# Kernel tuning notes

Measured on AMD Instinct MI355X. Metric: run time of the kernel, lower is better.

Reference implementation:

```python
import jax, jax.numpy as jnp
import numpy as np

B, S, D, DS, NSLOT = 2, 1024, 1024, 320, 512
H, CH = 4, 5
DFF = 4 * D
MAXIT = 2


def _ln(x, g, b, eps=1e-5):
    m = x.mean(-1, keepdims=True)
    v = ((x - m) ** 2).mean(-1, keepdims=True)
    return (x - m) * jax.lax.rsqrt(v + eps) * g + b


def _mha(x, Wq, Wk, Wv, Wo, bq, bk, bv, bo, nh):
    b_, s_, d_ = x.shape
    hd = d_ // nh
    q = (x @ Wq + bq).reshape(b_, s_, nh, hd)
    k = (x @ Wk + bk).reshape(b_, s_, nh, hd)
    v = (x @ Wv + bv).reshape(b_, s_, nh, hd)
    a = jax.nn.softmax(jnp.einsum('bqhd,bkhd->bhqk', q, k) * (hd ** -0.5), axis=-1)
    o = jnp.einsum('bhqk,bkhd->bqhd', a, v).reshape(b_, s_, d_)
    return o @ Wo + bo


def setup_inputs():
    key = jax.random.key(0)
    ks = iter(jax.random.split(key, 64))
    n = lambda shape: jax.random.normal(next(ks), shape, jnp.float32) * 0.02
    z = lambda shape: jnp.zeros(shape, jnp.float32)
    o = lambda shape: jnp.ones(shape, jnp.float32)
    return dict(
        x=jax.random.normal(next(ks), (B, S, D), jnp.float32),
        cache=jax.random.normal(next(ks), (B, NSLOT, DS), jnp.float32),
        iter_emb=n((16, D)),
        rq_w=n((D, D)), rg_w=n((D, 1)), rg_b=z((1,)), ck_w=n((DS, D)), cv_w=n((DS, D)),
        aq_w=n((D, D)), ak_w=n((D, D)), av_w=n((D, D)), ao_w=n((D, D)),
        aq_b=z((D,)), ak_b=z((D,)), av_b=z((D,)), ao_b=z((D,)),
        f1_w=n((D, DFF)), f1_b=z((DFF,)), f2_w=n((DFF, D)), f2_b=z((D,)),
        n1_g=o((D,)), n1_b=z((D,)), n2_g=o((D,)), n2_b=z((D,)),
        sq_w=n((DS, DS)), tk_w=n((D, DS)), tv_w=n((D, DS)), wg_w=n((D, 1)), wg_b=z((1,)),
        cq_w=n((DS, DS)), ck2_w=n((DS, DS)), cv2_w=n((DS, DS)), co_w=n((DS, DS)),
        cq_b=z((DS,)), ck2_b=z((DS,)), cv2_b=z((DS,)), co_b=z((DS,)),
        cn_g=o((DS,)), cn_b=z((DS,)),
        max_iterations=MAXIT,
    )


def reference(x, cache, iter_emb, rq_w, rg_w, rg_b, ck_w, cv_w,
              aq_w, ak_w, av_w, ao_w, aq_b, ak_b, av_b, ao_b,
              f1_w, f1_b, f2_w, f2_b, n1_g, n1_b, n2_g, n2_b,
              sq_w, tk_w, tv_w, wg_w, wg_b,
              cq_w, ck2_w, cv2_w, co_w, cq_b, ck2_b, cv2_b, co_b, cn_g, cn_b,
              max_iterations):
    def mem_read(h, cc):
        # gather from cache: gated cross-attention readout
        q = h @ rq_w                                   # [B,S,D]
        k = cc @ ck_w                                  # [B,N,D]
        v = cc @ cv_w                                  # [B,N,D]
        a = jax.nn.softmax(jnp.einsum('bsd,bnd->bsn', q, k) * (D ** -0.5), axis=-1)
        readout = jnp.einsum('bsn,bnd->bsd', a, v)
        gate = jax.nn.sigmoid(h @ rg_w + rg_b)          # [B,S,1] soft read gate
        return h + gate * readout

    def compute_block(h):
        # faithful to ComputeBlock (non-linear-attention branch): norm1 used twice
        hn = _ln(h, n1_g, n1_b)
        attn = _mha(hn, aq_w, ak_w, av_w, ao_w, aq_b, ak_b, av_b, ao_b, H)
        h = _ln(h + attn, n1_g, n1_b)
        ffn = jax.nn.gelu(h @ f1_w + f1_b) @ f2_w + f2_b
        return _ln(h + ffn, n2_g, n2_b)

    def mem_write(h, cc):
        # importance-scored scatter: slots attend over tokens, gated by importance
        sq = cc @ sq_w                                  # [B,N,DS]
        tk = h @ tk_w                                   # [B,S,DS]
        tv = h @ tv_w                                   # [B,S,DS]
        gate = jax.nn.sigmoid(h @ wg_w + wg_b)          # [B,S,1] soft write gate
        a = jax.nn.softmax(jnp.einsum('bnd,bsd->bns', sq, tk) * (DS ** -0.5), axis=-1)
        upd = jnp.einsum('bns,bsd->bnd', a, gate * tv)
        return cc + upd

    def cache_self_attn(cc):
        attn = _mha(cc, cq_w, ck2_w, cv2_w, co_w, cq_b, ck2_b, cv2_b, co_b, CH)
        return _ln(cc + attn, cn_g, cn_b)

    h = x
    cc = cache
    layer_input = x
    h_prev = None
    for it in range(max_iterations):
        h = h + iter_emb[it][None, None, :]
        if it > 0:
            h = h + layer_input + h_prev
        h_enh = mem_read(h, cc)
        h_comp = compute_block(h_enh)
        cc = mem_write(h_comp, cc)
        cc = cache_self_attn(cc)
        h = h_comp
        h_prev = jax.lax.stop_gradient(h_comp)  # torch: h_prev = h_computed.detach()
    return h
```

## Files before the change

### kernel.cpp

```cpp
#include <hip/hip_runtime.h>
#include <cstdint>

constexpr int B_ = 2, S_ = 1024, D_ = 1024, DS_ = 320, NSLOT_ = 512;
constexpr int H_ = 4, CH_ = 5, DFF_ = 4096;
constexpr int HD_ = D_ / H_;
constexpr int CHD_ = DS_ / CH_;
constexpr int BS_ = B_ * S_;
constexpr int BNS_ = B_ * NSLOT_;

typedef unsigned short u16;
typedef __attribute__((ext_vector_type(8))) short bf16x8;
typedef __attribute__((ext_vector_type(4))) float f32x4;
typedef __attribute__((ext_vector_type(4))) u16 u16x4;
typedef long long ll;

__device__ __forceinline__ u16 f2bf(float f) {
  unsigned u = __float_as_uint(f);
  return (u16)((u + 0x7FFFu + ((u >> 16) & 1u)) >> 16);
}
__device__ __forceinline__ float bf2f(u16 h) { return __uint_as_float((unsigned)h << 16); }

__device__ __forceinline__ void gload16(const void* g, void* l) {
  __builtin_amdgcn_global_load_lds((const __attribute__((address_space(1))) void*)g,
                                   (__attribute__((address_space(3))) void*)l, 16, 0, 0);
}

__global__ __launch_bounds__(512, 4)
void k_gemm(const u16* __restrict__ A, int lda, ll sA, ll sA2,
            const u16* __restrict__ Bp, int ldb, ll sB, ll sB2,
            float* __restrict__ outF, u16* __restrict__ outB,
            int ldc, ll sC, ll sC2,
            u16* __restrict__ outBT, int ldt, ll sT, ll sT2,
            int K, int zdiv, const float* __restrict__ bias,
            const float* __restrict__ rowscale, int rscfrom,
            int splitcol, int act)
{
  constexpr int ABYT = 128 * 128;
  constexpr int BBYT = 64 * 128;
  constexpr int BUF = ABYT + BBYT;
  const int z = blockIdx.z, zb = z / zdiv, zr = z - zb * zdiv;
  A  += (ll)zb * sA + (ll)zr * sA2;
  Bp += (ll)zb * sB + (ll)zr * sB2;
  const ll cof = (ll)zb * sC + (ll)zr * sC2;
  const ll tof = (ll)zb * sT + (ll)zr * sT2;
  const int bm = blockIdx.y * 128, bn = blockIdx.x * 64;
  __shared__ __align__(16) char lds[3 * BUF];
  const int tid = threadIdx.x;
  const int lane = tid & 63, wid = tid >> 6;
  const int rowb = wid * 16;

  f32x4 acc[4];
  const f32x4 fz = {0.f, 0.f, 0.f, 0.f};
  #pragma unroll
  for (int j = 0; j < 4; ++j) acc[j] = fz;

  const int trow = tid >> 3;
  const int tg   = ((tid & 7) ^ (trow & 7)) * 8;
  const u16* gA  = A + (ll)(bm + trow) * lda + tg;
  const u16* gA2 = gA + (ll)64 * lda;
  const u16* gB  = Bp + (ll)(bn + trow) * ldb + tg;

  const int r = lane & 15, q = lane >> 4;
  const int c7 = r & 7;
  const int gs0 = ((q) ^ c7) << 4;
  const int gs1 = ((4 + q) ^ c7) << 4;
  const int aoff = (rowb + r) * 128;
  int boff[4];
  #pragma unroll
  for (int j = 0; j < 4; ++j) boff[j] = ABYT + (j * 16 + r) * 128;

  auto stage = [&](int buf, int it) {
    char* la = lds + buf * BUF + wid * 1024;
    char* lb = la + ABYT;
    const int ko = it << 6;
    gload16(gA + ko, la);
    gload16(gA2 + ko, la + 8192);
    gload16(gB + ko, lb);
  };

  const int nsteps = K >> 6;
  stage(0, 0);
  if (nsteps > 1) stage(1, 1);
  for (int it = 0; it < nsteps; ++it) {
    if (it == nsteps - 1) asm volatile("s_waitcnt vmcnt(0)" ::: "memory");
    else                  asm volatile("s_waitcnt vmcnt(3)" ::: "memory");
    __builtin_amdgcn_s_barrier();
    __builtin_amdgcn_sched_barrier(0);
    if (it + 2 < nsteps) {
      int nb = it + 2; while (nb >= 3) nb -= 3;
      stage(nb, it + 2);
    }
    int p = it; while (p >= 3) p -= 3;
    const char* pa = lds + p * BUF;
    #pragma unroll
    for (int s = 0; s < 2; ++s) {
      const int gso = s ? gs1 : gs0;
      bf16x8 af = *(const bf16x8*)(pa + aoff + gso);
      bf16x8 bv[4];
      #pragma unroll
      for (int j = 0; j < 4; ++j) bv[j] = *(const bf16x8*)(pa + boff[j] + gso);
      #pragma unroll
      for (int j = 0; j < 4; ++j)
        acc[j] = __builtin_amdgcn_mfma_f32_16x16x32_bf16(af, bv[j], acc[j], 0, 0, 0);
    }
    asm volatile("s_waitcnt lgkmcnt(0)" ::: "memory");
    __builtin_amdgcn_sched_barrier(0);
  }

  const int fr = lane & 15, fq = lane >> 4;
  const int r0 = bm + rowb + fq * 4;
  #pragma unroll
  for (int j = 0; j < 4; ++j) {
    const int cn = bn + j * 16 + fr;
    const float bvv = bias ? bias[cn] : 0.f;
    const bool doRs = rowscale && (cn >= rscfrom);
    float vv[4];
    #pragma unroll
    for (int t = 0; t < 4; ++t) {
      float v = acc[j][t] + bvv;
      if (doRs) v *= rowscale[r0 + t];
      if (act) v = 0.5f * v * (1.f + tanhf(0.7978845608028654f * (v + 0.044715f * v * v * v)));
      vv[t] = v;
    }
    if (cn < splitcol) {
      if (outF) {
        #pragma unroll
        for (int t = 0; t < 4; ++t) outF[cof + (ll)(r0 + t) * ldc + cn] = vv[t];
      }
      if (outB) {
        #pragma unroll
        for (int t = 0; t < 4; ++t) outB[cof + (ll)(r0 + t) * ldc + cn] = f2bf(vv[t]);
      }
    } else {
      u16x4 pk = {f2bf(vv[0]), f2bf(vv[1]), f2bf(vv[2]), f2bf(vv[3])};
      *(u16x4*)(outBT + tof + (ll)(cn - splitcol) * ldt + r0) = pk;
    }
  }
}

struct PrepTable {
  const float* src[16];
  u16* dst[16];
  int R[16];
  int C[16];
  int off[17];
};

__global__ __launch_bounds__(256)
void k_prep_all(PrepTable T)
{
  __shared__ float t[32][33];
  const int b = blockIdx.x;
  int w = 0;
  #pragma unroll
  for (int i = 1; i < 16; ++i) if (b >= T.off[i]) w = i;
  const int lb = b - T.off[w];
  const int tilesC = T.C[w] >> 5;
  const int by = (lb / tilesC) << 5;
  const int bx = (lb - (lb / tilesC) * tilesC) << 5;
  const float* in = T.src[w];
  u16* out = T.dst[w];
  const int R = T.R[w], C = T.C[w];
  const int tx = threadIdx.x & 31, ty = threadIdx.x >> 5;
  #pragma unroll
  for (int i = 0; i < 32; i += 8)
    t[ty + i][tx] = in[(ll)(by + ty + i) * C + bx + tx];
  __syncthreads();
  #pragma unroll
  for (int i = 0; i < 32; i += 8)
    out[(ll)(bx + ty + i) * R + by + tx] = f2bf(t[tx][ty + i]);
}

__global__ __launch_bounds__(256)
void k_cvt(const float* __restrict__ in, u16* __restrict__ out, int n)
{
  int i = blockIdx.x * 256 + threadIdx.x;
  if (i < n) out[i] = f2bf(in[i]);
}

__global__ __launch_bounds__(256)
void k_cat3f(float* __restrict__ dst, const float* __restrict__ a, int na,
             const float* __restrict__ b, int nb, const float* __restrict__ c, int nc)
{
  int i = blockIdx.x * 256 + threadIdx.x;
  if (i < na) dst[i] = a[i];
  else if (i < na + nb) dst[i] = b[i - na];
  else if (i < na + nb + nc) dst[i] = c[i - na - nb];
}

__global__ __launch_bounds__(256)
void k_softmax_b16(u16* __restrict__ x, int cols, float scale)
{
  u16* p = x + (ll)blockIdx.x * cols;
  const int tid = threadIdx.x;
  __shared__ float red[256];
  float v[4];
  float m = -1e30f;
  #pragma unroll
  for (int i = 0; i < 4; ++i) {
    const int c = tid + (i << 8);
    v[i] = (c < cols) ? bf2f(p[c]) * scale : -1e30f;
    m = fmaxf(m, v[i]);
  }
  red[tid] = m; __syncthreads();
  for (int s = 128; s > 0; s >>= 1) { if (tid < s) red[tid] = fmaxf(red[tid], red[tid + s]); __syncthreads(); }
  m = red[0]; __syncthreads();
  float sum = 0.f;
  #pragma unroll
  for (int i = 0; i < 4; ++i) { v[i] = expf(v[i] - m); sum += v[i]; }
  red[tid] = sum; __syncthreads();
  for (int s = 128; s > 0; s >>= 1) { if (tid < s) red[tid] += red[tid + s]; __syncthreads(); }
  const float inv = 1.f / red[0];
  #pragma unroll
  for (int i = 0; i < 4; ++i) {
    const int c = tid + (i << 8);
    if (c < cols) p[c] = f2bf(v[i] * inv);
  }
}

__global__ __launch_bounds__(256)
void k_layernorm(const float* __restrict__ x, const float* __restrict__ res,
                 const float* __restrict__ res2, const float* __restrict__ rbias,
                 const float* __restrict__ g, const float* __restrict__ b,
                 float* __restrict__ outF, u16* __restrict__ outB, int cols)
{
  const ll ro = (ll)blockIdx.x * cols;
  const float* px = x + ro;
  const float* pr = res ? res + ro : nullptr;
  const float* p2 = res2 ? res2 + ro : nullptr;
  __shared__ float red[256];
  const int tid = threadIdx.x;
  auto val = [&](int c) {
    float v = px[c];
    if (pr) v += pr[c];
    if (p2) v += p2[c];
    if (rbias) v += rbias[c];
    return v;
  };
  float s = 0.f;
  for (int c = tid; c < cols; c += 256) s += val(c);
  red[tid] = s; __syncthreads();
  for (int t = 128; t > 0; t >>= 1) { if (tid < t) red[tid] += red[tid + t]; __syncthreads(); }
  const float mean = red[0] / cols; __syncthreads();
  float s2 = 0.f;
  for (int c = tid; c < cols; c += 256) { float v = val(c) - mean; s2 += v * v; }
  red[tid] = s2; __syncthreads();
  for (int t = 128; t > 0; t >>= 1) { if (tid < t) red[tid] += red[tid + t]; __syncthreads(); }
  const float inv = rsqrtf(red[0] / cols + 1e-5f);
  for (int c = tid; c < cols; c += 256) {
    float v = (val(c) - mean) * inv * g[c] + b[c];
    if (outF) outF[ro + c] = v;
    if (outB) outB[ro + c] = f2bf(v);
  }
}

__global__ __launch_bounds__(256)
void k_gate_add_ln(const float* __restrict__ h, const float* __restrict__ rr,
                   const float* __restrict__ w, const float* __restrict__ b0,
                   const float* __restrict__ g, const float* __restrict__ b,
                   float* __restrict__ outF, u16* __restrict__ outB)
{
  constexpr int C = 1024;
  const ll ro = (ll)blockIdx.x * C;
  const float* ph = h + ro;
  const float* pr = rr + ro;
  __shared__ float red[256];
  const int tid = threadIdx.x;
  float hv[4], rv[4];
  float s = 0.f;
  #pragma unroll
  for (int i = 0; i < 4; ++i) {
    const int c = tid + (i << 8);
    hv[i] = ph[c]; rv[i] = pr[c];
    s += hv[i] * w[c];
  }
  red[tid] = s; __syncthreads();
  for (int t = 128; t > 0; t >>= 1) { if (tid < t) red[tid] += red[tid + t]; __syncthreads(); }
  const float gate = 1.0f / (1.0f + expf(-(red[0] + b0[0])));
  __syncthreads();
  float vsum = 0.f;
  float vv[4];
  #pragma unroll
  for (int i = 0; i < 4; ++i) { vv[i] = hv[i] + gate * rv[i]; vsum += vv[i]; }
  red[tid] = vsum; __syncthreads();
  for (int t = 128; t > 0; t >>= 1) { if (tid < t) red[tid] += red[tid + t]; __syncthreads(); }
  const float mean = red[0] / C; __syncthreads();
  float v2 = 0.f;
  #pragma unroll
  for (int i = 0; i < 4; ++i) { float d = vv[i] - mean; v2 += d * d; }
  red[tid] = v2; __syncthreads();
  for (int t = 128; t > 0; t >>= 1) { if (tid < t) red[tid] += red[tid + t]; __syncthreads(); }
  const float inv = rsqrtf(red[0] / C + 1e-5f);
  #pragma unroll
  for (int i = 0; i < 4; ++i) {
    const int c = tid + (i << 8);
    outF[ro + c] = vv[i];
    outB[ro + c] = f2bf((vv[i] - mean) * inv * g[c] + b[c]);
  }
}

__global__ __launch_bounds__(256)
void k_gate(const float* __restrict__ x, const float* __restrict__ w,
            const float* __restrict__ b0, float* __restrict__ out, int cols)
{
  const int lane = threadIdx.x & 63;
  const int wv = threadIdx.x >> 6;
  const ll row = (ll)blockIdx.x * 4 + wv;
  const float* p = x + row * cols;
  float s = 0.f;
  for (int c = lane; c < cols; c += 64) s += p[c] * w[c];
  #pragma unroll
  for (int off = 32; off > 0; off >>= 1) s += __shfl_down(s, off);
  if (lane == 0) out[row] = 1.0f / (1.0f + expf(-(s + b0[0])));
}

__global__ __launch_bounds__(256)
void k_combine2(float* __restrict__ oF, u16* __restrict__ oB,
                const float* __restrict__ a, float sa, const float* __restrict__ b,
                const float* __restrict__ emb, int n, int Dm1)
{
  int i = blockIdx.x * 256 + threadIdx.x;
  if (i >= n) return;
  float v = sa * a[i];
  if (b) v += b[i];
  v += emb[i & Dm1];
  oF[i] = v; oB[i] = f2bf(v);
}

__global__ __launch_bounds__(256)
void k_add2(float* __restrict__ oF, u16* __restrict__ oB,
            const float* __restrict__ a, const float* __restrict__ b, int n)
{
  int i = blockIdx.x * 256 + threadIdx.x;
  if (i >= n) return;
  float v = a[i] + b[i];
  oF[i] = v; oB[i] = f2bf(v);
}

extern "C" void kernel_launch(void* const* d_in, const int* in_sizes, int n_in,
                              void* d_out, int out_size, void* d_ws, size_t ws_size,
                              hipStream_t stream)
{
  (void)in_sizes; (void)n_in; (void)out_size;
  const float* x        = (const float*)d_in[0];
  const float* cache0   = (const float*)d_in[1];
  const float* iter_emb = (const float*)d_in[2];
  const float* rq_w     = (const float*)d_in[3];
  const float* rg_w     = (const float*)d_in[4];
  const float* rg_b     = (const float*)d_in[5];
  const float* ck_w     = (const float*)d_in[6];
  const float* cv_w     = (const float*)d_in[7];
  const float* aq_w     = (const float*)d_in[8];
  const float* ak_w     = (const float*)d_in[9];
  const float* av_w     = (const float*)d_in[10];
  const float* ao_w     = (const float*)d_in[11];
  const float* aq_b     = (const float*)d_in[12];
  const float* ak_b     = (const float*)d_in[13];
  const float* av_b     = (const float*)d_in[14];
  const float* ao_b     = (const float*)d_in[15];
  const float* f1_w     = (const float*)d_in[16];
  const float* f1_b     = (const float*)d_in[17];
  const float* f2_w     = (const float*)d_in[18];
  const float* f2_b     = (const float*)d_in[19];
  const float* n1_g     = (const float*)d_in[20];
  const float* n1_b     = (const float*)d_in[21];
  const float* n2_g     = (const float*)d_in[22];
  const float* n2_b     = (const float*)d_in[23];
  const float* sq_w     = (const float*)d_in[24];
  const float* tk_w     = (const float*)d_in[25];
  const float* tv_w     = (const float*)d_in[26];
  const float* wg_w     = (const float*)d_in[27];
  const float* wg_b     = (const float*)d_in[28];
  const float* cq_w     = (const float*)d_in[29];
  const float* ck2_w    = (const float*)d_in[30];
  const float* cv2_w    = (const float*)d_in[31];
  const float* co_w     = (const float*)d_in[32];
  const float* cq_b     = (const float*)d_in[33];
  const float* ck2_b    = (const float*)d_in[34];
  const float* cv2_b    = (const float*)d_in[35];
  const float* co_b     = (const float*)d_in[36];
  const float* cn_g     = (const float*)d_in[37];
  const float* cn_b     = (const float*)d_in[38];

  float* out = (float*)d_out;

  size_t off = 0;
  char* base = (char*)d_ws;
  auto allocF = [&](size_t n) { float* p = (float*)(base + off); off += n * 4; off = (off + 255) & ~(size_t)255; return p; };
  auto allocH = [&](size_t n) { u16* p = (u16*)(base + off); off += n * 2; off = (off + 255) & ~(size_t)255; return p; };

  float* hbuf  = allocF((size_t)BS_ * D_);
  float* henh  = allocF((size_t)BS_ * D_);
  float* hcomp = allocF((size_t)BS_ * D_);
  float* h2b   = allocF((size_t)BS_ * D_);
  float* tA    = allocF((size_t)2 * BS_ * D_);
  float* gate  = allocF((size_t)BS_);
  float* ccnf  = allocF((size_t)BNS_ * DS_);
  float* updf  = allocF((size_t)BNS_ * DS_);
  float* coo   = allocF((size_t)BNS_ * DS_);
  float* ccwf  = allocF((size_t)BNS_ * DS_);
  float* qkvb  = allocF(3 * D_);
  float* cqkvb = allocF(3 * DS_);
  u16* rqT  = allocH((size_t)D_ * D_);
  u16* ckT  = allocH((size_t)D_ * DS_);
  u16* cvT  = allocH((size_t)D_ * DS_);
  u16* aqT  = allocH((size_t)D_ * D_);
  u16* akT  = allocH((size_t)D_ * D_);
  u16* avT  = allocH((size_t)D_ * D_);
  u16* aoT  = allocH((size_t)D_ * D_);
  u16* f1T  = allocH((size_t)DFF_ * D_);
  u16* f2T  = allocH((size_t)D_ * DFF_);
  u16* sqT  = allocH((size_t)DS_ * DS_);
  u16* tkT  = allocH((size_t)DS_ * D_);
  u16* tvTw = allocH((size_t)DS_ * D_);
  u16* cqT  = allocH((size_t)DS_ * DS_);
  u16* ck2T = allocH((size_t)DS_ * DS_);
  u16* cv2T = allocH((size_t)DS_ * DS_);
  u16* coT  = allocH((size_t)DS_ * DS_);
  u16* bb1  = allocH((size_t)BS_ * D_);
  u16* bb2  = allocH((size_t)BS_ * D_);
  u16* bb3  = allocH((size_t)BS_ * D_);
  u16* bb4  = allocH((size_t)BS_ * D_);
  u16* bb5  = allocH((size_t)B_ * H_ * S_ * S_);
  u16* bbQK = allocH((size_t)BS_ * 2 * D_);
  u16* bbCQK= allocH((size_t)BNS_ * 2 * DS_);
  u16* cc0b = allocH((size_t)BNS_ * DS_);
  u16* ccwb = allocH((size_t)BNS_ * DS_);
  u16* sqb  = allocH((size_t)BNS_ * DS_);
  u16* tkb  = allocH((size_t)BS_ * DS_);
  u16* tvTb = allocH((size_t)DS_ * BS_);
  u16* ccnb = allocH((size_t)BNS_ * DS_);
  u16* cv2Tb= allocH((size_t)DS_ * BNS_);
  u16* csab = allocH((size_t)BNS_ * DS_);
  if (off > ws_size) return;
  (void)cvT; (void)akT; (void)avT; (void)tvTw; (void)ck2T; (void)cv2T;

  auto gemm = [&](int M, int N, int K, int z, int zdiv,
                  const u16* Ap, int lda, ll sa, ll sa2,
                  const u16* Bq, int ldb, ll sb, ll sb2,
                  float* oF, u16* oB, int ldc, ll sc, ll sc2,
                  u16* oBT, int ldt, ll st, ll st2,
                  const float* bias, const float* rsc, int rscfrom,
                  int splitcol, int act) {
    dim3 g(N / 64, M / 128, z);
    k_gemm<<<g, 512, 0, stream>>>(Ap, lda, sa, sa2, Bq, ldb, sb, sb2,
        oF, oB, ldc, sc, sc2, oBT, ldt, st, st2, K, zdiv, bias, rsc, rscfrom, splitcol, act);
  };
  auto lnorm = [&](const float* xp, const float* rp, const float* rp2, const float* rb,
                   const float* g, const float* b, float* oF, u16* oB, int rows, int cols) {
    k_layernorm<<<rows, 256, 0, stream>>>(xp, rp, rp2, rb, g, b, oF, oB, cols);
  };
  auto eg = [](int n) { return dim3((n + 255) / 256); };

  {
    PrepTable T;
    const float* srcs[16] = {rq_w, ck_w, cv_w, aq_w, ak_w, av_w, ao_w, f1_w,
                             f2_w, sq_w, tk_w, tv_w, cq_w, ck2_w, cv2_w, co_w};
    u16* dsts[16] = {rqT, ckT, cvT, aqT, akT, avT, aoT, f1T,
                     f2T, sqT, tkT, tvTw, cqT, ck2T, cv2T, coT};
    const int Rs[16] = {D_, DS_, DS_, D_, D_, D_, D_, D_, DFF_, DS_, D_, D_, DS_, DS_, DS_, DS_};
    const int Cs[16] = {D_, D_, D_, D_, D_, D_, D_, DFF_, D_, DS_, DS_, DS_, DS_, DS_, DS_, DS_};
    int acc0 = 0;
    for (int i = 0; i < 16; ++i) {
      T.src[i] = srcs[i]; T.dst[i] = dsts[i]; T.R[i] = Rs[i]; T.C[i] = Cs[i];
      T.off[i] = acc0;
      acc0 += (Rs[i] >> 5) * (Cs[i] >> 5);
    }
    T.off[16] = acc0;
    k_prep_all<<<acc0, 256, 0, stream>>>(T);
  }
  k_cvt<<<eg(BNS_ * DS_), 256, 0, stream>>>(cache0, cc0b, BNS_ * DS_);
  k_cat3f<<<eg(3 * D_), 256, 0, stream>>>(qkvb, aq_b, D_, ak_b, D_, av_b, D_);
  k_cat3f<<<eg(3 * DS_), 256, 0, stream>>>(cqkvb, cq_b, DS_, ck2_b, DS_, cv2_b, DS_);

  auto mem_read = [&](const float* h_f, const u16* h_b, const u16* cc_b, float* o_henh) {
    gemm(BS_, D_, D_, 1, 1, h_b, D_, 0, 0, rqT, D_, 0, 0,
         nullptr, bb2, D_, 0, 0, nullptr, 0, 0, 0,
         nullptr, nullptr, 0, D_, 0);
    gemm(BNS_, 2 * D_, DS_, 1, 1, cc_b, DS_, 0, 0, ckT, DS_, 0, 0,
         nullptr, bb3, D_, 0, 0, bb4, BNS_, 0, 0,
         nullptr, nullptr, 0, D_, 0);
    gemm(S_, NSLOT_, D_, B_, 1, bb2, D_, (ll)S_ * D_, 0,
         bb3, D_, (ll)NSLOT_ * D_, 0,
         nullptr, bb5, NSLOT_, (ll)S_ * NSLOT_, 0, nullptr, 0, 0, 0,
         nullptr, nullptr, 0, NSLOT_, 0);
    k_softmax_b16<<<B_ * S_, 256, 0, stream>>>(bb5, NSLOT_, 0.03125f);
    gemm(S_, D_, NSLOT_, B_, 1, bb5, NSLOT_, (ll)S_ * NSLOT_, 0,
         bb4, BNS_, NSLOT_, 0,
         tA, nullptr, D_, (ll)S_ * D_, 0, nullptr, 0, 0, 0,
         nullptr, nullptr, 0, D_, 0);
    k_gate_add_ln<<<BS_, 256, 0, stream>>>(h_f, tA, rg_w, rg_b, n1_g, n1_b,
                                           o_henh, bb1);
  };

  auto compute_block = [&](const float* he, float* oF, u16* oB) {
    gemm(BS_, 3 * D_, D_, 1, 1, bb1, D_, 0, 0, aqT, D_, 0, 0,
         nullptr, bbQK, 2 * D_, 0, 0, bb4, BS_, 0, 0,
         qkvb, nullptr, 0, 2 * D_, 0);
    gemm(S_, S_, HD_, B_ * H_, H_,
         bbQK, 2 * D_, (ll)S_ * 2 * D_, HD_,
         bbQK + D_, 2 * D_, (ll)S_ * 2 * D_, HD_,
         nullptr, bb5, S_, (ll)H_ * S_ * S_, (ll)S_ * S_, nullptr, 0, 0, 0,
         nullptr, nullptr, 0, S_, 0);
    k_softmax_b16<<<B_ * H_ * S_, 256, 0, stream>>>(bb5, S_, 0.0625f);
    gemm(S_, HD_, S_, B_ * H_, H_,
         bb5, S_, (ll)H_ * S_ * S_, (ll)S_ * S_,
         bb4, BS_, S_, (ll)HD_ * BS_,
         nullptr, bb2, D_, (ll)S_ * D_, HD_, nullptr, 0, 0, 0,
         nullptr, nullptr, 0, HD_, 0);
    gemm(BS_, D_, D_, 1, 1, bb2, D_, 0, 0, aoT, D_, 0, 0,
         tA, nullptr, D_, 0, 0, nullptr, 0, 0, 0,
         ao_b, nullptr, 0, D_, 0);
    lnorm(he, tA, nullptr, nullptr, n1_g, n1_b, h2b, bb1, BS_, D_);
    gemm(BS_, DFF_, D_, 1, 1, bb1, D_, 0, 0, f1T, D_, 0, 0,
         nullptr, bb5, DFF_, 0, 0, nullptr, 0, 0, 0,
         f1_b, nullptr, 0, DFF_, 1);
    gemm(BS_, D_, 2048, 2, 2, bb5, DFF_, 0, 2048, f2T, DFF_, 0, 2048,
         tA, nullptr, D_, 0, (ll)BS_ * D_, nullptr, 0, 0, 0,
         nullptr, nullptr, 0, D_, 0);
    lnorm(h2b, tA, tA + (ll)BS_ * D_, f2_b, n2_g, n2_b, oF, oB, BS_, D_);
  };

  auto mem_write_csa = [&](const float* hc_f, const u16* hc_b,
                           const float* ccin_f, const u16* ccin_b) {
    gemm(BNS_, DS_, DS_, 1, 1, ccin_b, DS_, 0, 0, sqT, DS_, 0, 0,
         nullptr, sqb, DS_, 0, 0, nullptr, 0, 0, 0,
         nullptr, nullptr, 0, DS_, 0);
    k_gate<<<BS_ / 4, 256, 0, stream>>>(hc_f, wg_w, wg_b, gate, D_);
    gemm(BS_, 2 * DS_, D_, 1, 1, hc_b, D_, 0, 0, tkT, D_, 0, 0,
         nullptr, tkb, DS_, 0, 0, tvTb, BS_, 0, 0,
         nullptr, gate, DS_, DS_, 0);
    gemm(NSLOT_, S_, DS_, B_, 1, sqb, DS_, (ll)NSLOT_ * DS_, 0,
         tkb, DS_, (ll)S_ * DS_, 0,
         nullptr, bb5, S_, (ll)NSLOT_ * S_, 0, nullptr, 0, 0, 0,
         nullptr, nullptr, 0, S_, 0);
    k_softmax_b16<<<B_ * NSLOT_, 256, 0, stream>>>(bb5, S_, 0.05590169943749474f);
    gemm(NSLOT_, DS_, S_, B_, 1, bb5, S_, (ll)NSLOT_ * S_, 0,
         tvTb, BS_, S_, 0,
         updf, nullptr, DS_, (ll)NSLOT_ * DS_, 0, nullptr, 0, 0, 0,
         nullptr, nullptr, 0, DS_, 0);
    k_add2<<<eg(BNS_ * DS_), 256, 0, stream>>>(ccnf, ccnb, ccin_f, updf, BNS_ * DS_);
    gemm(BNS_, 3 * DS_, DS_, 1, 1, ccnb, DS_, 0, 0, cqT, DS_, 0, 0,
         nullptr, bbCQK, 2 * DS_, 0, 0, cv2Tb, BNS_, 0, 0,
         cqkvb, nullptr, 0, 2 * DS_, 0);
    gemm(NSLOT_, NSLOT_, CHD_, B_ * CH_, CH_,
         bbCQK, 2 * DS_, (ll)NSLOT_ * 2 * DS_, CHD_,
         bbCQK + DS_, 2 * DS_, (ll)NSLOT_ * 2 * DS_, CHD_,
         nullptr, bb5, NSLOT_, (ll)CH_ * NSLOT_ * NSLOT_, (ll)NSLOT_ * NSLOT_,
         nullptr, 0, 0, 0, nullptr, nullptr, 0, NSLOT_, 0);
    k_softmax_b16<<<B_ * CH_ * NSLOT_, 256, 0, stream>>>(bb5, NSLOT_, 0.125f);
    gemm(NSLOT_, CHD_, NSLOT_, B_ * CH_, CH_,
         bb5, NSLOT_, (ll)CH_ * NSLOT_ * NSLOT_, (ll)NSLOT_ * NSLOT_,
         cv2Tb, BNS_, NSLOT_, (ll)CHD_ * BNS_,
         nullptr, csab, DS_, (ll)NSLOT_ * DS_, CHD_, nullptr, 0, 0, 0,
         nullptr, nullptr, 0, CHD_, 0);
    gemm(BNS_, DS_, DS_, 1, 1, csab, DS_, 0, 0, coT, DS_, 0, 0,
         coo, nullptr, DS_, 0, 0, nullptr, 0, 0, 0,
         co_b, nullptr, 0, DS_, 0);
    lnorm(ccnf, coo, nullptr, nullptr, cn_g, cn_b, ccwf, ccwb, BNS_, DS_);
  };

  k_combine2<<<eg(BS_ * D_), 256, 0, stream>>>(hbuf, bb1, x, 1.0f, nullptr, iter_emb, BS_ * D_, D_ - 1);
  mem_read(hbuf, bb1, cc0b, henh);
  compute_block(henh, hcomp, bb3);
  mem_write_csa(hcomp, bb3, cache0, cc0b);

  k_combine2<<<eg(BS_ * D_), 256, 0, stream>>>(hbuf, bb1, hcomp, 2.0f, x, iter_emb + D_, BS_ * D_, D_ - 1);
  mem_read(hbuf, bb1, ccwb, henh);
  compute_block(henh, out, nullptr);
}
```

Before: 530.0 us.

## Shrink GEMM tile to 64x64 with double buffering and fuse residual add

The GEMM kernel moves from 128x64 tiles with 512 threads and a 3-stage LDS ring to 64x64 tiles with 256 threads and 2-stage double buffering. The waitcnt drops to vmcnt(0) every step. This raises the block count for the small-M GEMMs (512- and 1024-row problems) and lowers LDS per block, but each block reuses less data and overlaps less load with compute. Separately, the cache-update residual add (k_add2) is folded into the attention-output GEMM epilogue through a new addF pointer, which removes one kernel launch and one intermediate buffer.

```diff
diff --git a/kernel.cpp b/kernel.cpp
--- a/kernel.cpp
+++ b/kernel.cpp
@@ -25,7 +25,7 @@
                                    (__attribute__((address_space(3))) void*)l, 16, 0, 0);
 }
 
-__global__ __launch_bounds__(512, 4)
+__global__ __launch_bounds__(256, 5)
 void k_gemm(const u16* __restrict__ A, int lda, ll sA, ll sA2,
             const u16* __restrict__ Bp, int ldb, ll sB, ll sB2,
             float* __restrict__ outF, u16* __restrict__ outB,
@@ -33,9 +33,10 @@
             u16* __restrict__ outBT, int ldt, ll sT, ll sT2,
             int K, int zdiv, const float* __restrict__ bias,
             const float* __restrict__ rowscale, int rscfrom,
+            const float* __restrict__ addF,
             int splitcol, int act)
 {
-  constexpr int ABYT = 128 * 128;
+  constexpr int ABYT = 64 * 128;
   constexpr int BBYT = 64 * 128;
   constexpr int BUF = ABYT + BBYT;
   const int z = blockIdx.z, zb = z / zdiv, zr = z - zb * zdiv;
@@ -43,8 +44,8 @@
   Bp += (ll)zb * sB + (ll)zr * sB2;
   const ll cof = (ll)zb * sC + (ll)zr * sC2;
   const ll tof = (ll)zb * sT + (ll)zr * sT2;
-  const int bm = blockIdx.y * 128, bn = blockIdx.x * 64;
-  __shared__ __align__(16) char lds[3 * BUF];
+  const int bm = blockIdx.y * 64, bn = blockIdx.x * 64;
+  __shared__ __align__(16) char lds[2 * BUF];
   const int tid = threadIdx.x;
   const int lane = tid & 63, wid = tid >> 6;
   const int rowb = wid * 16;
@@ -57,8 +58,9 @@
   const int trow = tid >> 3;
   const int tg   = ((tid & 7) ^ (trow & 7)) * 8;
   const u16* gA  = A + (ll)(bm + trow) * lda + tg;
-  const u16* gA2 = gA + (ll)64 * lda;
+  const u16* gA2 = gA + (ll)32 * lda;
   const u16* gB  = Bp + (ll)(bn + trow) * ldb + tg;
+  const u16* gB2 = gB + (ll)32 * ldb;
 
   const int r = lane & 15, q = lane >> 4;
   const int c7 = r & 7;
@@ -74,24 +76,20 @@
     char* lb = la + ABYT;
     const int ko = it << 6;
     gload16(gA + ko, la);
-    gload16(gA2 + ko, la + 8192);
+    gload16(gA2 + ko, la + 4096);
     gload16(gB + ko, lb);
+    gload16(gB2 + ko, lb + 4096);
   };
 
   const int nsteps = K >> 6;
   stage(0, 0);
-  if (nsteps > 1) stage(1, 1);
+  int bufp = 0;
   for (int it = 0; it < nsteps; ++it) {
-    if (it == nsteps - 1) asm volatile("s_waitcnt vmcnt(0)" ::: "memory");
-    else                  asm volatile("s_waitcnt vmcnt(3)" ::: "memory");
+    asm volatile("s_waitcnt vmcnt(0)" ::: "memory");
     __builtin_amdgcn_s_barrier();
     __builtin_amdgcn_sched_barrier(0);
-    if (it + 2 < nsteps) {
-      int nb = it + 2; while (nb >= 3) nb -= 3;
-      stage(nb, it + 2);
-    }
-    int p = it; while (p >= 3) p -= 3;
-    const char* pa = lds + p * BUF;
+    if (it + 1 < nsteps) stage(bufp ^ 1, it + 1);
+    const char* pa = lds + bufp * BUF;
     #pragma unroll
     for (int s = 0; s < 2; ++s) {
       const int gso = s ? gs1 : gs0;
@@ -105,6 +103,7 @@
     }
     asm volatile("s_waitcnt lgkmcnt(0)" ::: "memory");
     __builtin_amdgcn_sched_barrier(0);
+    bufp ^= 1;
   }
 
   const int fr = lane & 15, fq = lane >> 4;
@@ -120,6 +119,7 @@
       float v = acc[j][t] + bvv;
       if (doRs) v *= rowscale[r0 + t];
       if (act) v = 0.5f * v * (1.f + tanhf(0.7978845608028654f * (v + 0.044715f * v * v * v)));
+      if (addF) v += addF[cof + (ll)(r0 + t) * ldc + cn];
       vv[t] = v;
     }
     if (cn < splitcol) {
@@ -324,16 +324,6 @@
   float v = sa * a[i];
   if (b) v += b[i];
   v += emb[i & Dm1];
-  oF[i] = v; oB[i] = f2bf(v);
-}
-
-__global__ __launch_bounds__(256)
-void k_add2(float* __restrict__ oF, u16* __restrict__ oB,
-            const float* __restrict__ a, const float* __restrict__ b, int n)
-{
-  int i = blockIdx.x * 256 + threadIdx.x;
-  if (i >= n) return;
-  float v = a[i] + b[i];
   oF[i] = v; oB[i] = f2bf(v);
 }
 
@@ -396,7 +386,6 @@
   float* tA    = allocF((size_t)2 * BS_ * D_);
   float* gate  = allocF((size_t)BS_);
   float* ccnf  = allocF((size_t)BNS_ * DS_);
-  float* updf  = allocF((size_t)BNS_ * DS_);
   float* coo   = allocF((size_t)BNS_ * DS_);
   float* ccwf  = allocF((size_t)BNS_ * DS_);
   float* qkvb  = allocF(3 * D_);
@@ -441,10 +430,11 @@
                   float* oF, u16* oB, int ldc, ll sc, ll sc2,
                   u16* oBT, int ldt, ll st, ll st2,
                   const float* bias, const float* rsc, int rscfrom,
-                  int splitcol, int act) {
-    dim3 g(N / 64, M / 128, z);
-    k_gemm<<<g, 512, 0, stream>>>(Ap, lda, sa, sa2, Bq, ldb, sb, sb2,
-        oF, oB, ldc, sc, sc2, oBT, ldt, st, st2, K, zdiv, bias, rsc, rscfrom, splitcol, act);
+                  const float* addF, int splitcol, int act) {
+    dim3 g(N / 64, M / 64, z);
+    k_gemm<<<g, 256, 0, stream>>>(Ap, lda, sa, sa2, Bq, ldb, sb, sb2,
+        oF, oB, ldc, sc, sc2, oBT, ldt, st, st2, K, zdiv, bias, rsc, rscfrom,
+        addF, splitcol, act);
   };
   auto lnorm = [&](const float* xp, const float* rp, const float* rp2, const float* rb,
                    const float* g, const float* b, float* oF, u16* oB, int rows, int cols) {
@@ -476,19 +466,19 @@
   auto mem_read = [&](const float* h_f, const u16* h_b, const u16* cc_b, float* o_henh) {
     gemm(BS_, D_, D_, 1, 1, h_b, D_, 0, 0, rqT, D_, 0, 0,
          nullptr, bb2, D_, 0, 0, nullptr, 0, 0, 0,
-         nullptr, nullptr, 0, D_, 0);
+         nullptr, nullptr, 0, nullptr, D_, 0);
     gemm(BNS_, 2 * D_, DS_, 1, 1, cc_b, DS_, 0, 0, ckT, DS_, 0, 0,
          nullptr, bb3, D_, 0, 0, bb4, BNS_, 0, 0,
-         nullptr, nullptr, 0, D_, 0);
+         nullptr, nullptr, 0, nullptr, D_, 0);
     gemm(S_, NSLOT_, D_, B_, 1, bb2, D_, (ll)S_ * D_, 0,
          bb3, D_, (ll)NSLOT_ * D_, 0,
          nullptr, bb5, NSLOT_, (ll)S_ * NSLOT_, 0, nullptr, 0, 0, 0,
-         nullptr, nullptr, 0, NSLOT_, 0);
+         nullptr, nullptr, 0, nullptr, NSLOT_, 0);
     k_softmax_b16<<<B_ * S_, 256, 0, stream>>>(bb5, NSLOT_, 0.03125f);
     gemm(S_, D_, NSLOT_, B_, 1, bb5, NSLOT_, (ll)S_ * NSLOT_, 0,
          bb4, BNS_, NSLOT_, 0,
          tA, nullptr, D_, (ll)S_ * D_, 0, nullptr, 0, 0, 0,
-         nullptr, nullptr, 0, D_, 0);
+         nullptr, nullptr, 0, nullptr, D_, 0);
     k_gate_add_ln<<<BS_, 256, 0, stream>>>(h_f, tA, rg_w, rg_b, n1_g, n1_b,
                                            o_henh, bb1);
   };
@@ -496,28 +486,28 @@
   auto compute_block = [&](const float* he, float* oF, u16* oB) {
     gemm(BS_, 3 * D_, D_, 1, 1, bb1, D_, 0, 0, aqT, D_, 0, 0,
          nullptr, bbQK, 2 * D_, 0, 0, bb4, BS_, 0, 0,
-         qkvb, nullptr, 0, 2 * D_, 0);
+         qkvb, nullptr, 0, nullptr, 2 * D_, 0);
     gemm(S_, S_, HD_, B_ * H_, H_,
          bbQK, 2 * D_, (ll)S_ * 2 * D_, HD_,
          bbQK + D_, 2 * D_, (ll)S_ * 2 * D_, HD_,
          nullptr, bb5, S_, (ll)H_ * S_ * S_, (ll)S_ * S_, nullptr, 0, 0, 0,
-         nullptr, nullptr, 0, S_, 0);
+         nullptr, nullptr, 0, nullptr, S_, 0);
     k_softmax_b16<<<B_ * H_ * S_, 256, 0, stream>>>(bb5, S_, 0.0625f);
     gemm(S_, HD_, S_, B_ * H_, H_,
          bb5, S_, (ll)H_ * S_ * S_, (ll)S_ * S_,
          bb4, BS_, S_, (ll)HD_ * BS_,
          nullptr, bb2, D_, (ll)S_ * D_, HD_, nullptr, 0, 0, 0,
-         nullptr, nullptr, 0, HD_, 0);
+         nullptr, nullptr, 0, nullptr, HD_, 0);
     gemm(BS_, D_, D_, 1, 1, bb2, D_, 0, 0, aoT, D_, 0, 0,
          tA, nullptr, D_, 0, 0, nullptr, 0, 0, 0,
-         ao_b, nullptr, 0, D_, 0);
+         ao_b, nullptr, 0, nullptr, D_, 0);
     lnorm(he, tA, nullptr, nullptr, n1_g, n1_b, h2b, bb1, BS_, D_);
     gemm(BS_, DFF_, D_, 1, 1, bb1, D_, 0, 0, f1T, D_, 0, 0,
          nullptr, bb5, DFF_, 0, 0, nullptr, 0, 0, 0,
-         f1_b, nullptr, 0, DFF_, 1);
+         f1_b, nullptr, 0, nullptr, DFF_, 1);
     gemm(BS_, D_, 2048, 2, 2, bb5, DFF_, 0, 2048, f2T, DFF_, 0, 2048,
          tA, nullptr, D_, 0, (ll)BS_ * D_, nullptr, 0, 0, 0,
-         nullptr, nullptr, 0, D_, 0);
+         nullptr, nullptr, 0, nullptr, D_, 0);
     lnorm(h2b, tA, tA + (ll)BS_ * D_, f2_b, n2_g, n2_b, oF, oB, BS_, D_);
   };
 
@@ -525,38 +515,37 @@
                            const float* ccin_f, const u16* ccin_b) {
     gemm(BNS_, DS_, DS_, 1, 1, ccin_b, DS_, 0, 0, sqT, DS_, 0, 0,
          nullptr, sqb, DS_, 0, 0, nullptr, 0, 0, 0,
-         nullptr, nullptr, 0, DS_, 0);
+         nullptr, nullptr, 0, nullptr, DS_, 0);
     k_gate<<<BS_ / 4, 256, 0, stream>>>(hc_f, wg_w, wg_b, gate, D_);
     gemm(BS_, 2 * DS_, D_, 1, 1, hc_b, D_, 0, 0, tkT, D_, 0, 0,
          nullptr, tkb, DS_, 0, 0, tvTb, BS_, 0, 0,
-         nullptr, gate, DS_, DS_, 0);
+         nullptr, gate, DS_, nullptr, DS_, 0);
     gemm(NSLOT_, S_, DS_, B_, 1, sqb, DS_, (ll)NSLOT_ * DS_, 0,
          tkb, DS_, (ll)S_ * DS_, 0,
          nullptr, bb5, S_, (ll)NSLOT_ * S_, 0, nullptr, 0, 0, 0,
-         nullptr, nullptr, 0, S_, 0);
+         nullptr, nullptr, 0, nullptr, S_, 0);
     k_softmax_b16<<<B_ * NSLOT_, 256, 0, stream>>>(bb5, S_, 0.05590169943749474f);
     gemm(NSLOT_, DS_, S_, B_, 1, bb5, S_, (ll)NSLOT_ * S_, 0,
          tvTb, BS_, S_, 0,
-         updf, nullptr, DS_, (ll)NSLOT_ * DS_, 0, nullptr, 0, 0, 0,
-         nullptr, nullptr, 0, DS_, 0);
-    k_add2<<<eg(BNS_ * DS_), 256, 0, stream>>>(ccnf, ccnb, ccin_f, updf, BNS_ * DS_);
+         ccnf, ccnb, DS_, (ll)NSLOT_ * DS_, 0, nullptr, 0, 0, 0,
+         nullptr, nullptr, 0, ccin_f, DS_, 0);
     gemm(BNS_, 3 * DS_, DS_, 1, 1, ccnb, DS_, 0, 0, cqT, DS_, 0, 0,
          nullptr, bbCQK, 2 * DS_, 0, 0, cv2Tb, BNS_, 0, 0,
-         cqkvb, nullptr, 0, 2 * DS_, 0);
+         cqkvb, nullptr, 0, nullptr, 2 * DS_, 0);
     gemm(NSLOT_, NSLOT_, CHD_, B_ * CH_, CH_,
          bbCQK, 2 * DS_, (ll)NSLOT_ * 2 * DS_, CHD_,
          bbCQK + DS_, 2 * DS_, (ll)NSLOT_ * 2 * DS_, CHD_,
          nullptr, bb5, NSLOT_, (ll)CH_ * NSLOT_ * NSLOT_, (ll)NSLOT_ * NSLOT_,
-         nullptr, 0, 0, 0, nullptr, nullptr, 0, NSLOT_, 0);
+         nullptr, 0, 0, 0, nullptr, nullptr, 0, nullptr, NSLOT_, 0);
     k_softmax_b16<<<B_ * CH_ * NSLOT_, 256, 0, stream>>>(bb5, NSLOT_, 0.125f);
     gemm(NSLOT_, CHD_, NSLOT_, B_ * CH_, CH_,
          bb5, NSLOT_, (ll)CH_ * NSLOT_ * NSLOT_, (ll)NSLOT_ * NSLOT_,
          cv2Tb, BNS_, NSLOT_, (ll)CHD_ * BNS_,
          nullptr, csab, DS_, (ll)NSLOT_ * DS_, CHD_, nullptr, 0, 0, 0,
-         nullptr, nullptr, 0, CHD_, 0);
+         nullptr, nullptr, 0, nullptr, CHD_, 0);
     gemm(BNS_, DS_, DS_, 1, 1, csab, DS_, 0, 0, coT, DS_, 0, 0,
          coo, nullptr, DS_, 0, 0, nullptr, 0, 0, 0,
-         co_b, nullptr, 0, DS_, 0);
+         co_b, nullptr, 0, nullptr, DS_, 0);
     lnorm(ccnf, coo, nullptr, nullptr, cn_g, cn_b, ccwf, ccwb, BNS_, DS_);
   };
 
```

After: 562.7 us. +6.2%, slower.
